# Optimization experiments

Measured on AMD Instinct MI355X. Metric: run time of the kernel, lower is better.

Reference implementation:

```python
import jax, jax.numpy as jnp
from jax import lax
import numpy as np

IMGSIZE = (360, 640)  # (H, W)
SIGMA = 71.0
LEVEL = 5
FACTOR = 2.0

_k1 = np.array([1., 4., 6., 4., 1.], dtype=np.float32) / 16.0
K5 = np.outer(_k1, _k1)  # 5x5 binomial (Gaussian) pyramid kernel


def _blur(x, scale=1.0):
    # x: (B,C,H,W); depthwise 5x5 Gaussian blur with reflect padding
    C = x.shape[1]
    xp = jnp.pad(x, ((0, 0), (0, 0), (2, 2), (2, 2)), mode='reflect')
    k = jnp.broadcast_to(jnp.asarray(K5 * scale, x.dtype), (C, 1, 5, 5))
    return lax.conv_general_dilated(xp, k, (1, 1), 'VALID',
                                    feature_group_count=C,
                                    dimension_numbers=('NCHW', 'OIHW', 'NCHW'))


def pyrdown(x):
    # OpenCV-style pyrDown: blur then drop every other row/col -> ceil(H/2), ceil(W/2)
    return _blur(x)[:, :, ::2, ::2]


def pyrup(x):
    # OpenCV-style pyrUp: zero-insertion upsample then blur with 4*kernel
    B, C, H, W = x.shape
    up = jnp.zeros((B, C, 2 * H, 2 * W), x.dtype).at[:, :, ::2, ::2].set(x)
    return _blur(up, scale=4.0)


def resize_nearest(x, h, w):
    # matches torch F.interpolate(mode='nearest'): src = floor(dst * in/out)
    H, W = x.shape[-2], x.shape[-1]
    ri = jnp.arange(h) * H // h
    ci = jnp.arange(w) * W // w
    return x[..., ri[:, None], ci[None, :]]


def _create_filter(height, width, sigma):
    s = 2.0 * sigma * sigma
    xc = int(round(width * 0.5))
    yc = int(round(height * 0.5))
    ex = jnp.arange(-xc, width - xc - 1, dtype=jnp.float32)   # (W-1,)
    ey = jnp.arange(-yc, height - yc - 1, dtype=jnp.float32)  # (H-1,)
    d = ex[:, None] ** 2 + ey[None, :] ** 2                   # (W-1, H-1)
    g = jnp.exp(-d / s)
    return (g / g.max()).T                                    # (H-1, W-1)


def _pyramid_filters():
    f = _create_filter(int(FACTOR * IMGSIZE[0]), int(FACTOR * IMGSIZE[1]), SIGMA)
    filters = [f]
    for _ in range(LEVEL):
        filters.append(pyrdown(filters[-1][None, None])[0, 0])
    return filters


def setup_inputs():
    key = jax.random.key(0)
    k1, k2 = jax.random.split(key)
    B, C = 32, 3
    H, W = IMGSIZE
    images = jax.random.normal(k1, (B, C, H, W), jnp.float32)
    u = jax.random.uniform(k2, (B, 2), jnp.float32)
    # fixations are (x, y) pixel coordinates inside the image
    fixations = u * jnp.array([W - 1.0, H - 1.0], jnp.float32)
    return {"images": images, "fixations": fixations}


def reference(images, fixations):
    filters = _pyramid_filters()
    # Laplacian pyramid construction
    pyr, cur = [], images
    up = images
    for _ in range(LEVEL):
        dn = pyrdown(cur)
        up = resize_nearest(pyrup(dn), cur.shape[2], cur.shape[3])
        pyr.append(cur - up)
        cur = dn
    fovea = up  # smallest level, upsampled back (im_smallest)
    for i in range(LEVEL - 1, -1, -1):
        f = filters[i]
        fh, fw = f.shape
        ih, iw = pyr[i].shape[2], pyr[i].shape[3]
        fix = fixations / (2.0 ** i)
        # rect = filter_size/2 - fix, truncated to int (same as torch .to(int64))
        x1 = (fw / 2.0 - fix[:, 0]).astype(jnp.int32)
        y1 = (fh / 2.0 - fix[:, 1]).astype(jnp.int32)
        # per-sample dynamic crop of size (ih, iw); crop size == target size so
        # the original's F.interpolate on the crop is the identity
        crop = jax.vmap(lambda yy, xx: lax.dynamic_slice(f, (yy, xx), (ih, iw)))(y1, x1)
        filtered = pyr[i] * crop[:, None, :, :]
        if i != LEVEL - 1:
            fovea = resize_nearest(pyrup(fovea), ih, iw)
        fovea = fovea + filtered
    return fovea
```

## Files before the change

kernel.cpp:

```cpp
#include <hip/hip_runtime.h>
#include <cstddef>


static __device__ __forceinline__ int refl(int e, int n) {
  if (e < 0) e = -e;
  if (e >= n) e = 2 * n - 2 - e;
  return e;
}

static __device__ __forceinline__ float4 loadu4(const float* p) {
  float4 v; __builtin_memcpy(&v, p, sizeof(float4)); return v;
}

static __device__ void filt_build(float* pool, float* __restrict__ fyg,
                                  float* __restrict__ fxg) {
  float* sy = pool;
  float* sx = pool + 1394;
  const int oy[5] = {0, 719, 1079, 1259, 1349};
  const int ny[5] = {719, 360, 180, 90, 45};
  const int ox[5] = {0, 1279, 1919, 2239, 2399};
  const int nx[5] = {1279, 640, 320, 160, 80};
  int tid = threadIdx.y * 64 + threadIdx.x;
  for (int i = tid; i < 719; i += 256) {
    float d = (float)(i - 360); sy[i] = expf(-d * d / 10082.0f);
  }
  for (int i = tid; i < 1279; i += 256) {
    float d = (float)(i - 640); sx[i] = expf(-d * d / 10082.0f);
  }
  __syncthreads();
  const float k0 = 0.0625f, k1 = 0.25f, k2 = 0.375f;
#pragma unroll
  for (int l = 1; l < 5; ++l) {
    const float* py = sy + oy[l - 1]; float* qy = sy + oy[l];
    int n = ny[l - 1];
    for (int i = tid; i < ny[l]; i += 256) {
      qy[i] = k0 * (py[refl(2 * i - 2, n)] + py[refl(2 * i + 2, n)]) +
              k1 * (py[refl(2 * i - 1, n)] + py[refl(2 * i + 1, n)]) +
              k2 * py[2 * i];
    }
    const float* px = sx + ox[l - 1]; float* qx = sx + ox[l];
    int m = nx[l - 1];
    for (int i = tid; i < nx[l]; i += 256) {
      qx[i] = k0 * (px[refl(2 * i - 2, m)] + px[refl(2 * i + 2, m)]) +
              k1 * (px[refl(2 * i - 1, m)] + px[refl(2 * i + 1, m)]) +
              k2 * px[2 * i];
    }
    __syncthreads();
  }
  for (int i = tid; i < 1394; i += 256) fyg[i] = sy[i];
  for (int i = tid; i < 2479; i += 256) fxg[i] = sx[i];
}

__global__ __launch_bounds__(256) void pyrdown_lds_k(
    const float* __restrict__ src, float* __restrict__ dst,
    int H, int W, int oH, int oW, int NP,
    float* __restrict__ fyo, float* __restrict__ fxo) {
  __shared__ float pool[35 * 68 * 2];
  int tx = threadIdx.x;
  int ty = threadIdx.y;
  int p  = blockIdx.z;
  if (p >= NP) {
    if (blockIdx.x == 0 && blockIdx.y == 0 && fyo) filt_build(pool, fyo, fxo);
    return;
  }
  float* te = pool;
  float* to_ = pool + 35 * 68;
  int x0 = blockIdx.x * 64;
  int Yb = blockIdx.y;
  const float* s = src + (size_t)p * H * W;
  float* d = dst + (size_t)p * oH * oW;

  int cols = min(64, oW - x0);
  int nq   = (cols + 4) >> 1;
  int gr0  = 32 * Yb - 2;
  int gc0  = 2 * x0 - 4;
  int tid  = ty * 64 + tx;

  auto loadq = [&](int r, int m) -> float4 {
    int gy = refl(gr0 + r, H);
    const float* row = s + (size_t)gy * W;
    int gc = gc0 + 4 * m;
    if (gc >= 0 && gc + 3 < W) return *(const float4*)(row + gc);
    float4 v;
    v.x = row[refl(gc, W)];
    v.y = row[refl(gc + 1, W)];
    v.z = row[refl(gc + 2, W)];
    v.w = row[refl(gc + 3, W)];
    return v;
  };
  auto putq = [&](int r, int m, float4 v) {
    *(float2*)&te[r * 68 + 2 * m]  = make_float2(v.x, v.z);
    *(float2*)&to_[r * 68 + 2 * m] = make_float2(v.y, v.w);
  };

  if (nq == 34) {
    int r0 = tid / 34,          m0 = tid - 34 * r0;
    int q1 = tid + 256;  int r1 = q1 / 34, m1 = q1 - 34 * r1;
    int q2 = tid + 512;  int r2 = q2 / 34, m2 = q2 - 34 * r2;
    int q3 = tid + 768;  int r3 = q3 / 34, m3 = q3 - 34 * r3;
    int q4 = tid + 1024; int r4 = q4 / 34, m4 = q4 - 34 * r4;
    bool g4 = (q4 < 1190);
    float4 v0 = loadq(r0, m0);
    float4 v1 = loadq(r1, m1);
    float4 v2 = loadq(r2, m2);
    float4 v3 = loadq(r3, m3);
    float4 v4;
    if (g4) v4 = loadq(r4, m4);
    putq(r0, m0, v0);
    putq(r1, m1, v1);
    putq(r2, m2, v2);
    putq(r3, m3, v3);
    if (g4) putq(r4, m4, v4);
  } else {
    float4 v[9];
#pragma unroll
    for (int i = 0; i < 9; ++i) {
      int r = ty + 4 * i;
      if (r < 35 && tx < nq) v[i] = loadq(r, tx);
    }
#pragma unroll
    for (int i = 0; i < 9; ++i) {
      int r = ty + 4 * i;
      if (r < 35 && tx < nq) putq(r, tx, v[i]);
    }
  }
  __syncthreads();

  int x = x0 + tx;
  int nPairs = (oH + 1) >> 1;
  int Yp0 = 8 * Yb + 2 * ty;
  if (x < oW && Yp0 < nPairs) {
    const float k0 = 0.0625f, k1 = 0.25f, k2 = 0.375f;
    float h[11];
    int rbase = 8 * ty;
#pragma unroll
    for (int a = 0; a < 11; ++a) {
      int r = rbase + a;
      float e0 = te[r * 68 + tx + 1], e2 = te[r * 68 + tx + 2],
            e4 = te[r * 68 + tx + 3];
      float e1 = to_[r * 68 + tx + 1], e3 = to_[r * 68 + tx + 2];
      h[a] = k0 * (e0 + e4) + k1 * (e1 + e3) + k2 * e2;
    }
    float o0 = k0 * (h[0] + h[4])  + k1 * (h[1] + h[3])  + k2 * h[2];
    float o1 = k0 * (h[2] + h[6])  + k1 * (h[3] + h[5])  + k2 * h[4];
    float o2 = k0 * (h[4] + h[8])  + k1 * (h[5] + h[7])  + k2 * h[6];
    float o3 = k0 * (h[6] + h[10]) + k1 * (h[7] + h[9])  + k2 * h[8];
    int oy0 = 2 * Yp0;
    float* drow = d + (size_t)oy0 * oW + x;
    drow[0] = o0;
    if (oy0 + 1 < oH) drow[(size_t)oW] = o1;
    if (oy0 + 2 < oH) drow[(size_t)2 * oW] = o2;
    if (oy0 + 3 < oH) drow[(size_t)3 * oW] = o3;
  }
}

static __device__ __forceinline__ float pyrdown_at(const float* c, int H, int W,
                                                   int y, int x) {
  const float k0 = 0.0625f, k1 = 0.25f, k2 = 0.375f;
  int c0 = refl(2 * x - 2, W), c1 = refl(2 * x - 1, W), c2 = 2 * x,
      c3 = refl(2 * x + 1, W), c4 = refl(2 * x + 2, W);
  float h[5];
#pragma unroll
  for (int r = 0; r < 5; ++r) {
    int gy = refl(2 * y - 2 + r, H);
    const float* row = c + gy * W;
    h[r] = k0 * (row[c0] + row[c4]) + k1 * (row[c1] + row[c3]) + k2 * row[c2];
  }
  return k0 * (h[0] + h[4]) + k1 * (h[1] + h[3]) + k2 * h[2];
}

static __device__ __forceinline__ float pyrup_at(const float* c, int Hc, int Wc,
                                                 int y, int x) {
  const float w0 = 0.125f, w1 = 0.75f;
  int yc = y >> 1, xc = x >> 1;
  if (y & 1) {
    int yb = (yc == Hc - 1) ? Hc - 1 : yc + 1;
    const float* ra = c + yc * Wc;
    const float* rb = c + yb * Wc;
    if (x & 1) {
      int xb = (xc == Wc - 1) ? Wc - 1 : xc + 1;
      return 0.25f * (ra[xc] + ra[xb] + rb[xc] + rb[xb]);
    } else {
      int xm = (xc == 0) ? 1 : xc - 1, xp = (xc == Wc - 1) ? Wc - 1 : xc + 1;
      float a = w1 * ra[xc] + w0 * (ra[xm] + ra[xp]);
      float b = w1 * rb[xc] + w0 * (rb[xm] + rb[xp]);
      return 0.5f * (a + b);
    }
  } else {
    int ym = (yc == 0) ? 1 : yc - 1, yp = (yc == Hc - 1) ? Hc - 1 : yc + 1;
    const float* rm = c + ym * Wc;
    const float* rc = c + yc * Wc;
    const float* rp = c + yp * Wc;
    if (x & 1) {
      int xb = (xc == Wc - 1) ? Wc - 1 : xc + 1;
      float a = 0.5f * (rm[xc] + rm[xb]);
      float b = 0.5f * (rc[xc] + rc[xb]);
      float e = 0.5f * (rp[xc] + rp[xb]);
      return w1 * b + w0 * (a + e);
    } else {
      int xm = (xc == 0) ? 1 : xc - 1, xp = (xc == Wc - 1) ? Wc - 1 : xc + 1;
      float a = w1 * rm[xc] + w0 * (rm[xm] + rm[xp]);
      float b = w1 * rc[xc] + w0 * (rc[xm] + rc[xp]);
      float e = w1 * rp[xc] + w0 * (rp[xm] + rp[xp]);
      return w1 * b + w0 * (a + e);
    }
  }
}

__global__ __launch_bounds__(256) void tail_k(
    const float* __restrict__ dn3, const float* __restrict__ fix,
    const float* __restrict__ fy3, const float* __restrict__ fx3,
    const float* __restrict__ fy4, const float* __restrict__ fx4,
    float* __restrict__ fv3) {
  __shared__ float c3[45 * 80];
  __shared__ float c4[23 * 40];
  __shared__ float c5[12 * 20];
  __shared__ float g4[23 * 40];
  int p = blockIdx.x;
  int tid = threadIdx.x;
  const float* src = dn3 + (size_t)p * 3600;
  for (int i = tid; i < 900; i += 256)
    ((float4*)c3)[i] = ((const float4*)src)[i];
  __syncthreads();
  for (int i = tid; i < 23 * 40; i += 256) {
    int y = i / 40, x = i - 40 * y;
    c4[i] = pyrdown_at(c3, 45, 80, y, x);
  }
  __syncthreads();
  for (int i = tid; i < 12 * 20; i += 256) {
    int y = i / 20, x = i - 20 * y;
    c5[i] = pyrdown_at(c4, 23, 40, y, x);
  }
  __syncthreads();
  int b = p / 3;
  float fxv = fix[2 * b + 0], fyv = fix[2 * b + 1];
  {
    int x1 = (int)(40.0f - fxv * 0.0625f);
    int y1 = (int)(22.5f - fyv * 0.0625f);
    for (int i = tid; i < 23 * 40; i += 256) {
      int y = i / 40, x = i - 40 * y;
      float u = pyrup_at(c5, 12, 20, y, x);
      g4[i] = u + (c4[i] - u) * (fy4[y1 + y] * fx4[x1 + x]);
    }
  }
  __syncthreads();
  {
    int x1 = (int)(80.0f - fxv * 0.125f);
    int y1 = (int)(45.0f - fyv * 0.125f);
    float* dst = fv3 + (size_t)p * 3600;
    for (int i = tid; i < 45 * 80; i += 256) {
      int y = i / 80, x = i - 80 * y;
      float uf = pyrup_at(g4, 23, 40, y, x);
      float ud = pyrup_at(c4, 23, 40, y, x);
      dst[i] = uf + (c3[i] - ud) * (fy3[y1 + y] * fx3[x1 + x]);
    }
  }
}

__global__ __launch_bounds__(256) void recon_fused_k(
    const float* __restrict__ images, const float* __restrict__ dn1,
    const float* __restrict__ dn2, const float* __restrict__ dn3,
    const float* __restrict__ fv3g, const float* __restrict__ fyg,
    const float* __restrict__ fxg, const float* __restrict__ fix,
    float* __restrict__ out) {
  __shared__ float dn1t[670], fv1t[670];
  __shared__ float dn2t[296], fv2t[296];
  __shared__ float dn3t[126], fv3t[126];
  const int bx = blockIdx.x, by = blockIdx.y, p = blockIdx.z;
  const int tid = threadIdx.x;

  const int R1r = max(8 * by - 1, 0),  R1hi = min(8 * by + 8, 179);
  const int C1r = max(64 * bx - 1, 0), C1hi = min(64 * bx + 64, 319);
  const int n1r = R1hi - R1r + 1, n1c = C1hi - C1r + 1;
  const int yc_lo = R1r >> 1, yc_hi = R1hi >> 1;
  const int xc_lo = C1r >> 1, xc_hi = C1hi >> 1;
  const int R2r = max(yc_lo - 1, 0),  R2hi = min(yc_hi + 1, 89);
  const int C2r = max(xc_lo - 1, 0),  C2hi = min(xc_hi + 1, 159);
  const int n2r = R2hi - R2r + 1, n2c = C2hi - C2r + 1;
  const int yc3_lo = R2r >> 1, yc3_hi = R2hi >> 1;
  const int xc3_lo = C2r >> 1, xc3_hi = C2hi >> 1;
  const int R3r = max(yc3_lo - 1, 0), R3hi = min(yc3_hi + 1, 44);
  const int C3r = max(xc3_lo - 1, 0), C3hi = min(xc3_hi + 1, 79);
  const int n3r = R3hi - R3r + 1, n3c = C3hi - C3r + 1;

  const float* d1p = dn1 + (size_t)p * 57600;
  const float* d2p = dn2 + (size_t)p * 14400;
  const float* d3p = dn3 + (size_t)p * 3600;
  const float* f3p = fv3g + (size_t)p * 3600;

  for (int s = tid; s < 670; s += 256) {
    int r = s / 67, c = s - 67 * r;
    if (r < n1r && c < n1c)
      dn1t[s] = d1p[(R1r + r) * 320 + (C1r + c)];
  }
  for (int s = tid; s < 296; s += 256) {
    int r = s / 37, c = s - 37 * r;
    if (r < n2r && c < n2c)
      dn2t[s] = d2p[(R2r + r) * 160 + (C2r + c)];
  }
  if (tid < 126) {
    int r = tid / 21, c = tid - 21 * r;
    if (r < n3r && c < n3c) {
      int o = (R3r + r) * 80 + (C3r + c);
      dn3t[tid] = d3p[o];
      fv3t[tid] = f3p[o];
    }
  }
  __syncthreads();

  int b = p / 3;
  float fxv = fix[2 * b + 0], fyv = fix[2 * b + 1];
  int y1_2 = (int)(90.0f - fyv * 0.25f), x1_2 = (int)(160.0f - fxv * 0.25f);
  int y1_1 = (int)(180.0f - fyv * 0.5f), x1_1 = (int)(320.0f - fxv * 0.5f);
  int y1_0 = (int)(359.5f - fyv),        x1_0 = (int)(639.5f - fxv);
  const float* fy2 = fyg + 1079; const float* fx2 = fxg + 1919;
  const float* fy1 = fyg + 719;  const float* fx1 = fxg + 1279;
  const float w0 = 0.125f, w1 = 0.75f;

  {
    int nx3 = xc3_hi - xc3_lo + 1;
    int ncell = (yc3_hi - yc3_lo + 1) * nx3;
    if (tid < ncell) {
      int cy = tid / nx3;
      int yc = yc3_lo + cy, xc = xc3_lo + (tid - cy * nx3);
      int aa0 = ((yc == 0) ? 1 : yc - 1) - R3r;
      int aa1 = yc - R3r;
      int aa2 = ((yc == 44) ? 44 : yc + 1) - R3r;
      int xm = ((xc == 0) ? 1 : xc - 1) - C3r;
      int xq = xc - C3r;
      int xp = ((xc == 79) ? 79 : xc + 1) - C3r;
      int aa[3] = {aa0, aa1, aa2};
      float heF[3], hoF[3], heD[3], hoD[3];
#pragma unroll
      for (int j = 0; j < 3; ++j) {
        const float* rf = fv3t + aa[j] * 21;
        float fm = rf[xm], fc = rf[xq], fp = rf[xp];
        heF[j] = w1 * fc + w0 * (fm + fp);
        hoF[j] = 0.5f * (fc + fp);
        const float* rd = dn3t + aa[j] * 21;
        float em = rd[xm], ec = rd[xq], ep = rd[xp];
        heD[j] = w1 * ec + w0 * (em + ep);
        hoD[j] = 0.5f * (ec + ep);
      }
      float uF[4] = {w1 * heF[1] + w0 * (heF[0] + heF[2]),
                     w1 * hoF[1] + w0 * (hoF[0] + hoF[2]),
                     0.5f * (heF[1] + heF[2]),
                     0.5f * (hoF[1] + hoF[2])};
      float uD[4] = {w1 * heD[1] + w0 * (heD[0] + heD[2]),
                     w1 * hoD[1] + w0 * (hoD[0] + hoD[2]),
                     0.5f * (heD[1] + heD[2]),
                     0.5f * (hoD[1] + hoD[2])};
      int y2 = 2 * yc, x2 = 2 * xc;
#pragma unroll
      for (int q = 0; q < 4; ++q) {
        int y = y2 + (q >> 1), x = x2 + (q & 1);
        if (y >= R2r && y <= R2hi && x >= C2r && x <= C2hi) {
          int idx = (y - R2r) * 37 + (x - C2r);
          float w = fy2[y1_2 + y] * fx2[x1_2 + x];
          fv2t[idx] = uF[q] + (dn2t[idx] - uD[q]) * w;
        }
      }
    }
  }
  __syncthreads();

  {
    int nx2 = xc_hi - xc_lo + 1;
    int ncell = (yc_hi - yc_lo + 1) * nx2;
    if (tid < ncell) {
      int cy = tid / nx2;
      int yc = yc_lo + cy, xc = xc_lo + (tid - cy * nx2);
      int aa0 = ((yc == 0) ? 1 : yc - 1) - R2r;
      int aa1 = yc - R2r;
      int aa2 = ((yc == 89) ? 89 : yc + 1) - R2r;
      int xm = ((xc == 0) ? 1 : xc - 1) - C2r;
      int xq = xc - C2r;
      int xp = ((xc == 159) ? 159 : xc + 1) - C2r;
      int aa[3] = {aa0, aa1, aa2};
      float heF[3], hoF[3], heD[3], hoD[3];
#pragma unroll
      for (int j = 0; j < 3; ++j) {
        const float* rf = fv2t + aa[j] * 37;
        float fm = rf[xm], fc = rf[xq], fp = rf[xp];
        heF[j] = w1 * fc + w0 * (fm + fp);
        hoF[j] = 0.5f * (fc + fp);
        const float* rd = dn2t + aa[j] * 37;
        float em = rd[xm], ec = rd[xq], ep = rd[xp];
        heD[j] = w1 * ec + w0 * (em + ep);
        hoD[j] = 0.5f * (ec + ep);
      }
      float uF[4] = {w1 * heF[1] + w0 * (heF[0] + heF[2]),
                     w1 * hoF[1] + w0 * (hoF[0] + hoF[2]),
                     0.5f * (heF[1] + heF[2]),
                     0.5f * (hoF[1] + hoF[2])};
      float uD[4] = {w1 * heD[1] + w0 * (heD[0] + heD[2]),
                     w1 * hoD[1] + w0 * (hoD[0] + hoD[2]),
                     0.5f * (heD[1] + heD[2]),
                     0.5f * (hoD[1] + hoD[2])};
      int y2 = 2 * yc, x2 = 2 * xc;
#pragma unroll
      for (int q = 0; q < 4; ++q) {
        int y = y2 + (q >> 1), x = x2 + (q & 1);
        if (y >= R1r && y <= R1hi && x >= C1r && x <= C1hi) {
          int idx = (y - R1r) * 67 + (x - C1r);
          float w = fy1[y1_1 + y] * fx1[x1_1 + x];
          fv1t[idx] = uF[q] + (dn1t[idx] - uD[q]) * w;
        }
      }
    }
  }
  __syncthreads();

  int trow = tid >> 5;
  int tk   = tid & 31;
  int Y = 8 * by + trow;
  if (Y >= 180) return;
  int c0 = 64 * bx + 2 * tk;
  int ry[3];
  ry[0] = ((Y == 0) ? 1 : Y - 1) - R1r;
  ry[1] = Y - R1r;
  ry[2] = ((Y == 179) ? 179 : Y + 1) - R1r;
  int cm = ((c0 == 0) ? 1 : c0 - 1) - C1r;
  int cc = c0 - C1r;
  int cp = ((c0 + 2 >= 320) ? 319 : c0 + 2) - C1r;

  float dm[3], da[3], db[3], dq[3], em[3], ea[3], eb[3], eq[3];
#pragma unroll
  for (int r = 0; r < 3; ++r) {
    const float* qd = dn1t + ry[r] * 67;
    dm[r] = qd[cm]; da[r] = qd[cc]; db[r] = qd[cc + 1]; dq[r] = qd[cp];
    const float* qe = fv1t + ry[r] * 67;
    em[r] = qe[cm]; ea[r] = qe[cc]; eb[r] = qe[cc + 1]; eq[r] = qe[cp];
  }

  float heA[3], hoA[3], heB[3], hoB[3];
#pragma unroll
  for (int r = 0; r < 3; ++r) {
    heA[r] = w1 * da[r] + w0 * (dm[r] + db[r]);
    hoA[r] = 0.5f * (da[r] + db[r]);
    heB[r] = w1 * db[r] + w0 * (da[r] + dq[r]);
    hoB[r] = 0.5f * (db[r] + dq[r]);
  }
  float u00 = w1 * heA[1] + w0 * (heA[0] + heA[2]);
  float u01 = w1 * hoA[1] + w0 * (hoA[0] + hoA[2]);
  float u02 = w1 * heB[1] + w0 * (heB[0] + heB[2]);
  float u03 = w1 * hoB[1] + w0 * (hoB[0] + hoB[2]);
  float u10 = 0.5f * (heA[1] + heA[2]);
  float u11 = 0.5f * (hoA[1] + hoA[2]);
  float u12 = 0.5f * (heB[1] + heB[2]);
  float u13 = 0.5f * (hoB[1] + hoB[2]);

  float geA[3], goA[3], geB[3], goB[3];
#pragma unroll
  for (int r = 0; r < 3; ++r) {
    geA[r] = w1 * ea[r] + w0 * (em[r] + eb[r]);
    goA[r] = 0.5f * (ea[r] + eb[r]);
    geB[r] = w1 * eb[r] + w0 * (ea[r] + eq[r]);
    goB[r] = 0.5f * (eb[r] + eq[r]);
  }
  float f00 = w1 * geA[1] + w0 * (geA[0] + geA[2]);
  float f01 = w1 * goA[1] + w0 * (goA[0] + goA[2]);
  float f02 = w1 * geB[1] + w0 * (geB[0] + geB[2]);
  float f03 = w1 * goB[1] + w0 * (goB[0] + goB[2]);
  float f10 = 0.5f * (geA[1] + geA[2]);
  float f11 = 0.5f * (goA[1] + goA[2]);
  float f12 = 0.5f * (geB[1] + geB[2]);
  float f13 = 0.5f * (goB[1] + goB[2]);

  int oy = 2 * Y, ox = 2 * c0;
  const float* crow = images + (size_t)p * 230400 + (size_t)oy * 640 + ox;
  float* orow = out + (size_t)p * 230400 + (size_t)oy * 640 + ox;
  float fyA = fyg[y1_0 + oy], fyB = fyg[y1_0 + oy + 1];
  float4 fxq = loadu4(fxg + (x1_0 + ox));

  float4 cv = *(const float4*)crow;
  float4 r0v;
  r0v.x = f00 + (cv.x - u00) * (fyA * fxq.x);
  r0v.y = f01 + (cv.y - u01) * (fyA * fxq.y);
  r0v.z = f02 + (cv.z - u02) * (fyA * fxq.z);
  r0v.w = f03 + (cv.w - u03) * (fyA * fxq.w);
  *(float4*)orow = r0v;
  float4 cv1 = *(const float4*)(crow + 640);
  float4 r1v;
  r1v.x = f10 + (cv1.x - u10) * (fyB * fxq.x);
  r1v.y = f11 + (cv1.y - u11) * (fyB * fxq.y);
  r1v.z = f12 + (cv1.z - u12) * (fyB * fxq.z);
  r1v.w = f13 + (cv1.w - u13) * (fyB * fxq.w);
  *(float4*)(orow + 640) = r1v;
}

extern "C" void kernel_launch(void* const* d_in, const int* in_sizes, int n_in,
                              void* d_out, int out_size, void* d_ws, size_t ws_size,
                              hipStream_t stream) {
  const float* images = (const float*)d_in[0];
  const float* fix    = (const float*)d_in[1];
  float* out = (float*)d_out;
  float* ws  = (float*)d_ws;

  const int P = 96;

  size_t off = 0;
  auto alloc = [&](size_t n) { float* p = ws + off; off += (n + 3) & ~(size_t)3; return p; };
  float* fyg = alloc(1394);
  float* fxg = alloc(2479);
  float* dn1 = alloc((size_t)P * 180 * 320);
  float* dn2 = alloc((size_t)P * 90 * 160);
  float* dn3 = alloc((size_t)P * 45 * 80);
  float* fv3 = alloc((size_t)P * 45 * 80);
  if (ws_size < off * sizeof(float)) return;

  dim3 blk(64, 4, 1);
  auto pgrd = [](int oW, int oH, int p) {
    int nPairs = (oH + 1) / 2;
    return dim3((unsigned)((oW + 63) / 64), (unsigned)((nPairs + 7) / 8), (unsigned)p);
  };

  pyrdown_lds_k<<<pgrd(320, 180, P + 1), blk, 0, stream>>>(
      images, dn1, 360, 640, 180, 320, P, fyg, fxg);
  pyrdown_lds_k<<<pgrd(160, 90, P), blk, 0, stream>>>(
      dn1, dn2, 180, 320, 90, 160, P, nullptr, nullptr);
  pyrdown_lds_k<<<pgrd(80, 45, P), blk, 0, stream>>>(
      dn2, dn3, 90, 160, 45, 80, P, nullptr, nullptr);

  tail_k<<<dim3(P), dim3(256), 0, stream>>>(
      dn3, fix, fyg + 1259, fxg + 2239, fyg + 1349, fxg + 2399, fv3);

  recon_fused_k<<<dim3(5, 23, P), dim3(256), 0, stream>>>(
      images, dn1, dn2, dn3, fv3, fyg, fxg, fix, out);
}
```

Baseline: 231.7 us.

## Fuse third pyrdown into tail kernel and enlarge recon tiles to 32 rows

The third pyramid-down level is now computed inside tail_k from dn2 staged in LDS, which removes one kernel launch and a global round trip. Each recon_fused_k block now covers 32 level-1 rows instead of 8, so halo overlap is smaller and there are fewer blocks. Each thread walks 4 rows with a sliding three-row register window, and global loads are batched into registers before the LDS writes. In exchange, tail_k uses about 74KB of LDS with only 96 blocks, which serialises work on few CUs, and recon has far fewer blocks.

```diff
diff --git a/kernel.cpp b/kernel.cpp
--- a/kernel.cpp
+++ b/kernel.cpp
@@ -208,19 +208,28 @@
 }
 
 __global__ __launch_bounds__(256) void tail_k(
-    const float* __restrict__ dn3, const float* __restrict__ fix,
+    const float* __restrict__ dn2g, const float* __restrict__ fix,
     const float* __restrict__ fy3, const float* __restrict__ fx3,
     const float* __restrict__ fy4, const float* __restrict__ fx4,
-    float* __restrict__ fv3) {
+    float* __restrict__ dn3g, float* __restrict__ fv3) {
+  __shared__ float s2[90 * 160];
   __shared__ float c3[45 * 80];
   __shared__ float c4[23 * 40];
   __shared__ float c5[12 * 20];
   __shared__ float g4[23 * 40];
   int p = blockIdx.x;
   int tid = threadIdx.x;
-  const float* src = dn3 + (size_t)p * 3600;
-  for (int i = tid; i < 900; i += 256)
-    ((float4*)c3)[i] = ((const float4*)src)[i];
+  const float* src = dn2g + (size_t)p * 14400;
+  for (int i = tid; i < 3600; i += 256)
+    ((float4*)s2)[i] = ((const float4*)src)[i];
+  __syncthreads();
+  float* d3 = dn3g + (size_t)p * 3600;
+  for (int i = tid; i < 3600; i += 256) {
+    int y = i / 80, x = i - 80 * y;
+    float v = pyrdown_at(s2, 90, 160, y, x);
+    c3[i] = v;
+    d3[i] = v;
+  }
   __syncthreads();
   for (int i = tid; i < 23 * 40; i += 256) {
     int y = i / 40, x = i - 40 * y;
@@ -263,14 +272,14 @@
     const float* __restrict__ fv3g, const float* __restrict__ fyg,
     const float* __restrict__ fxg, const float* __restrict__ fix,
     float* __restrict__ out) {
-  __shared__ float dn1t[670], fv1t[670];
-  __shared__ float dn2t[296], fv2t[296];
-  __shared__ float dn3t[126], fv3t[126];
+  __shared__ float dn1t[2278], fv1t[2278];
+  __shared__ float dn2t[740],  fv2t[740];
+  __shared__ float dn3t[252],  fv3t[252];
   const int bx = blockIdx.x, by = blockIdx.y, p = blockIdx.z;
   const int tid = threadIdx.x;
 
-  const int R1r = max(8 * by - 1, 0),  R1hi = min(8 * by + 8, 179);
-  const int C1r = max(64 * bx - 1, 0), C1hi = min(64 * bx + 64, 319);
+  const int R1r = max(32 * by - 1, 0),  R1hi = min(32 * by + 32, 179);
+  const int C1r = max(64 * bx - 1, 0),  C1hi = min(64 * bx + 64, 319);
   const int n1r = R1hi - R1r + 1, n1c = C1hi - C1r + 1;
   const int yc_lo = R1r >> 1, yc_hi = R1hi >> 1;
   const int xc_lo = C1r >> 1, xc_hi = C1hi >> 1;
@@ -288,23 +297,45 @@
   const float* d3p = dn3 + (size_t)p * 3600;
   const float* f3p = fv3g + (size_t)p * 3600;
 
-  for (int s = tid; s < 670; s += 256) {
-    int r = s / 67, c = s - 67 * r;
-    if (r < n1r && c < n1c)
-      dn1t[s] = d1p[(R1r + r) * 320 + (C1r + c)];
-  }
-  for (int s = tid; s < 296; s += 256) {
-    int r = s / 37, c = s - 37 * r;
-    if (r < n2r && c < n2c)
-      dn2t[s] = d2p[(R2r + r) * 160 + (C2r + c)];
-  }
-  if (tid < 126) {
-    int r = tid / 21, c = tid - 21 * r;
-    if (r < n3r && c < n3c) {
-      int o = (R3r + r) * 80 + (C3r + c);
-      dn3t[tid] = d3p[o];
-      fv3t[tid] = f3p[o];
-    }
+  {
+    float v1[9];
+#pragma unroll
+    for (int it = 0; it < 9; ++it) {
+      int s = tid + 256 * it;
+      if (s < 2278) {
+        int r = s / 67, c = s - 67 * r;
+        if (r < n1r && c < n1c) v1[it] = d1p[(R1r + r) * 320 + (C1r + c)];
+      }
+    }
+    float v2[3];
+#pragma unroll
+    for (int it = 0; it < 3; ++it) {
+      int s = tid + 256 * it;
+      if (s < 740) {
+        int r = s / 37, c = s - 37 * r;
+        if (r < n2r && c < n2c) v2[it] = d2p[(R2r + r) * 160 + (C2r + c)];
+      }
+    }
+    float v3a = 0.f, v3b = 0.f;
+    if (tid < 252) {
+      int r = tid / 21, c = tid - 21 * r;
+      if (r < n3r && c < n3c) {
+        int o = (R3r + r) * 80 + (C3r + c);
+        v3a = d3p[o];
+        v3b = f3p[o];
+      }
+    }
+#pragma unroll
+    for (int it = 0; it < 9; ++it) {
+      int s = tid + 256 * it;
+      if (s < 2278) dn1t[s] = v1[it];
+    }
+#pragma unroll
+    for (int it = 0; it < 3; ++it) {
+      int s = tid + 256 * it;
+      if (s < 740) dn2t[s] = v2[it];
+    }
+    if (tid < 252) { dn3t[tid] = v3a; fv3t[tid] = v3b; }
   }
   __syncthreads();
 
@@ -318,18 +349,18 @@
   const float w0 = 0.125f, w1 = 0.75f;
 
   {
-    int nx3 = xc3_hi - xc3_lo + 1;
-    int ncell = (yc3_hi - yc3_lo + 1) * nx3;
+    int nxa = xc3_hi - xc3_lo + 1;
+    int ncell = (yc3_hi - yc3_lo + 1) * nxa;
     if (tid < ncell) {
-      int cy = tid / nx3;
-      int yc = yc3_lo + cy, xc = xc3_lo + (tid - cy * nx3);
-      int aa0 = ((yc == 0) ? 1 : yc - 1) - R3r;
-      int aa1 = yc - R3r;
-      int aa2 = ((yc == 44) ? 44 : yc + 1) - R3r;
+      int cy = tid / nxa;
+      int yc = yc3_lo + cy, xc = xc3_lo + (tid - cy * nxa);
+      int a0 = ((yc == 0) ? 1 : yc - 1) - R3r;
+      int a1 = yc - R3r;
+      int a2 = ((yc == 44) ? 44 : yc + 1) - R3r;
       int xm = ((xc == 0) ? 1 : xc - 1) - C3r;
       int xq = xc - C3r;
       int xp = ((xc == 79) ? 79 : xc + 1) - C3r;
-      int aa[3] = {aa0, aa1, aa2};
+      int aa[3] = {a0, a1, a2};
       float heF[3], hoF[3], heD[3], hoD[3];
 #pragma unroll
       for (int j = 0; j < 3; ++j) {
@@ -365,18 +396,18 @@
   __syncthreads();
 
   {
-    int nx2 = xc_hi - xc_lo + 1;
-    int ncell = (yc_hi - yc_lo + 1) * nx2;
-    if (tid < ncell) {
-      int cy = tid / nx2;
-      int yc = yc_lo + cy, xc = xc_lo + (tid - cy * nx2);
-      int aa0 = ((yc == 0) ? 1 : yc - 1) - R2r;
-      int aa1 = yc - R2r;
-      int aa2 = ((yc == 89) ? 89 : yc + 1) - R2r;
+    int nxb = xc_hi - xc_lo + 1;
+    int ncell = (yc_hi - yc_lo + 1) * nxb;
+    for (int s = tid; s < ncell; s += 256) {
+      int cy = s / nxb;
+      int yc = yc_lo + cy, xc = xc_lo + (s - cy * nxb);
+      int a0 = ((yc == 0) ? 1 : yc - 1) - R2r;
+      int a1 = yc - R2r;
+      int a2 = ((yc == 89) ? 89 : yc + 1) - R2r;
       int xm = ((xc == 0) ? 1 : xc - 1) - C2r;
       int xq = xc - C2r;
       int xp = ((xc == 159) ? 159 : xc + 1) - C2r;
-      int aa[3] = {aa0, aa1, aa2};
+      int aa[3] = {a0, a1, a2};
       float heF[3], hoF[3], heD[3], hoD[3];
 #pragma unroll
       for (int j = 0; j < 3; ++j) {
@@ -411,82 +442,80 @@
   }
   __syncthreads();
 
-  int trow = tid >> 5;
-  int tk   = tid & 31;
-  int Y = 8 * by + trow;
-  if (Y >= 180) return;
+  int tg = tid >> 5;
+  int tk = tid & 31;
+  int Y0 = 32 * by + 4 * tg;
+  if (Y0 > 179) return;
   int c0 = 64 * bx + 2 * tk;
-  int ry[3];
-  ry[0] = ((Y == 0) ? 1 : Y - 1) - R1r;
-  ry[1] = Y - R1r;
-  ry[2] = ((Y == 179) ? 179 : Y + 1) - R1r;
   int cm = ((c0 == 0) ? 1 : c0 - 1) - C1r;
   int cc = c0 - C1r;
   int cp = ((c0 + 2 >= 320) ? 319 : c0 + 2) - C1r;
 
-  float dm[3], da[3], db[3], dq[3], em[3], ea[3], eb[3], eq[3];
-#pragma unroll
-  for (int r = 0; r < 3; ++r) {
-    const float* qd = dn1t + ry[r] * 67;
-    dm[r] = qd[cm]; da[r] = qd[cc]; db[r] = qd[cc + 1]; dq[r] = qd[cp];
-    const float* qe = fv1t + ry[r] * 67;
-    em[r] = qe[cm]; ea[r] = qe[cc]; eb[r] = qe[cc + 1]; eq[r] = qe[cp];
-  }
-
-  float heA[3], hoA[3], heB[3], hoB[3];
-#pragma unroll
-  for (int r = 0; r < 3; ++r) {
-    heA[r] = w1 * da[r] + w0 * (dm[r] + db[r]);
-    hoA[r] = 0.5f * (da[r] + db[r]);
-    heB[r] = w1 * db[r] + w0 * (da[r] + dq[r]);
-    hoB[r] = 0.5f * (db[r] + dq[r]);
-  }
-  float u00 = w1 * heA[1] + w0 * (heA[0] + heA[2]);
-  float u01 = w1 * hoA[1] + w0 * (hoA[0] + hoA[2]);
-  float u02 = w1 * heB[1] + w0 * (heB[0] + heB[2]);
-  float u03 = w1 * hoB[1] + w0 * (hoB[0] + hoB[2]);
-  float u10 = 0.5f * (heA[1] + heA[2]);
-  float u11 = 0.5f * (hoA[1] + hoA[2]);
-  float u12 = 0.5f * (heB[1] + heB[2]);
-  float u13 = 0.5f * (hoB[1] + hoB[2]);
-
-  float geA[3], goA[3], geB[3], goB[3];
-#pragma unroll
-  for (int r = 0; r < 3; ++r) {
-    geA[r] = w1 * ea[r] + w0 * (em[r] + eb[r]);
-    goA[r] = 0.5f * (ea[r] + eb[r]);
-    geB[r] = w1 * eb[r] + w0 * (ea[r] + eq[r]);
-    goB[r] = 0.5f * (eb[r] + eq[r]);
-  }
-  float f00 = w1 * geA[1] + w0 * (geA[0] + geA[2]);
-  float f01 = w1 * goA[1] + w0 * (goA[0] + goA[2]);
-  float f02 = w1 * geB[1] + w0 * (geB[0] + geB[2]);
-  float f03 = w1 * goB[1] + w0 * (goB[0] + goB[2]);
-  float f10 = 0.5f * (geA[1] + geA[2]);
-  float f11 = 0.5f * (goA[1] + goA[2]);
-  float f12 = 0.5f * (geB[1] + geB[2]);
-  float f13 = 0.5f * (goB[1] + goB[2]);
-
-  int oy = 2 * Y, ox = 2 * c0;
-  const float* crow = images + (size_t)p * 230400 + (size_t)oy * 640 + ox;
-  float* orow = out + (size_t)p * 230400 + (size_t)oy * 640 + ox;
-  float fyA = fyg[y1_0 + oy], fyB = fyg[y1_0 + oy + 1];
+  struct Hrow { float dAe, dAo, dBe, dBo, fAe, fAo, fBe, fBo; };
+  auto loadrow = [&](int j) -> Hrow {
+    int rr = Y0 - 1 + j;
+    rr = (rr < 0) ? 1 : (rr > 179 ? 179 : rr);
+    const float* qd = dn1t + (rr - R1r) * 67;
+    const float* qe = fv1t + (rr - R1r) * 67;
+    float d0 = qd[cm], d1 = qd[cc], d2 = qd[cc + 1], d3v = qd[cp];
+    float e0 = qe[cm], e1 = qe[cc], e2 = qe[cc + 1], e3v = qe[cp];
+    Hrow h;
+    h.dAe = w1 * d1 + w0 * (d0 + d2);  h.dAo = 0.5f * (d1 + d2);
+    h.dBe = w1 * d2 + w0 * (d1 + d3v); h.dBo = 0.5f * (d2 + d3v);
+    h.fAe = w1 * e1 + w0 * (e0 + e2);  h.fAo = 0.5f * (e1 + e2);
+    h.fBe = w1 * e2 + w0 * (e1 + e3v); h.fBo = 0.5f * (e2 + e3v);
+    return h;
+  };
+
+  Hrow hp = loadrow(0), hc = loadrow(1), hn = loadrow(2);
+  int ox = 2 * c0;
+  const float* ibase = images + (size_t)p * 230400 + ox;
+  float* obase = out + (size_t)p * 230400 + ox;
   float4 fxq = loadu4(fxg + (x1_0 + ox));
 
-  float4 cv = *(const float4*)crow;
-  float4 r0v;
-  r0v.x = f00 + (cv.x - u00) * (fyA * fxq.x);
-  r0v.y = f01 + (cv.y - u01) * (fyA * fxq.y);
-  r0v.z = f02 + (cv.z - u02) * (fyA * fxq.z);
-  r0v.w = f03 + (cv.w - u03) * (fyA * fxq.w);
-  *(float4*)orow = r0v;
-  float4 cv1 = *(const float4*)(crow + 640);
-  float4 r1v;
-  r1v.x = f10 + (cv1.x - u10) * (fyB * fxq.x);
-  r1v.y = f11 + (cv1.y - u11) * (fyB * fxq.y);
-  r1v.z = f12 + (cv1.z - u12) * (fyB * fxq.z);
-  r1v.w = f13 + (cv1.w - u13) * (fyB * fxq.w);
-  *(float4*)(orow + 640) = r1v;
+#pragma unroll
+  for (int i = 0; i < 4; ++i) {
+    int Y = Y0 + i;
+    if (Y <= 179) {
+      float u00 = w1 * hc.dAe + w0 * (hp.dAe + hn.dAe);
+      float u01 = w1 * hc.dAo + w0 * (hp.dAo + hn.dAo);
+      float u02 = w1 * hc.dBe + w0 * (hp.dBe + hn.dBe);
+      float u03 = w1 * hc.dBo + w0 * (hp.dBo + hn.dBo);
+      float u10 = 0.5f * (hc.dAe + hn.dAe);
+      float u11 = 0.5f * (hc.dAo + hn.dAo);
+      float u12 = 0.5f * (hc.dBe + hn.dBe);
+      float u13 = 0.5f * (hc.dBo + hn.dBo);
+      float f00 = w1 * hc.fAe + w0 * (hp.fAe + hn.fAe);
+      float f01 = w1 * hc.fAo + w0 * (hp.fAo + hn.fAo);
+      float f02 = w1 * hc.fBe + w0 * (hp.fBe + hn.fBe);
+      float f03 = w1 * hc.fBo + w0 * (hp.fBo + hn.fBo);
+      float f10 = 0.5f * (hc.fAe + hn.fAe);
+      float f11 = 0.5f * (hc.fAo + hn.fAo);
+      float f12 = 0.5f * (hc.fBe + hn.fBe);
+      float f13 = 0.5f * (hc.fBo + hn.fBo);
+
+      int oy = 2 * Y;
+      const float* crow = ibase + (size_t)oy * 640;
+      float* orow = obase + (size_t)oy * 640;
+      float fyA = fyg[y1_0 + oy], fyB = fyg[y1_0 + oy + 1];
+
+      float4 cv = *(const float4*)crow;
+      float4 r0v;
+      r0v.x = f00 + (cv.x - u00) * (fyA * fxq.x);
+      r0v.y = f01 + (cv.y - u01) * (fyA * fxq.y);
+      r0v.z = f02 + (cv.z - u02) * (fyA * fxq.z);
+      r0v.w = f03 + (cv.w - u03) * (fyA * fxq.w);
+      *(float4*)orow = r0v;
+      float4 cv1 = *(const float4*)(crow + 640);
+      float4 r1v;
+      r1v.x = f10 + (cv1.x - u10) * (fyB * fxq.x);
+      r1v.y = f11 + (cv1.y - u11) * (fyB * fxq.y);
+      r1v.z = f12 + (cv1.z - u12) * (fyB * fxq.z);
+      r1v.w = f13 + (cv1.w - u13) * (fyB * fxq.w);
+      *(float4*)(orow + 640) = r1v;
+    }
+    if (i < 3) { hp = hc; hc = hn; hn = loadrow(i + 3); }
+  }
 }
 
 extern "C" void kernel_launch(void* const* d_in, const int* in_sizes, int n_in,
@@ -519,12 +548,10 @@
       images, dn1, 360, 640, 180, 320, P, fyg, fxg);
   pyrdown_lds_k<<<pgrd(160, 90, P), blk, 0, stream>>>(
       dn1, dn2, 180, 320, 90, 160, P, nullptr, nullptr);
-  pyrdown_lds_k<<<pgrd(80, 45, P), blk, 0, stream>>>(
-      dn2, dn3, 90, 160, 45, 80, P, nullptr, nullptr);
 
   tail_k<<<dim3(P), dim3(256), 0, stream>>>(
-      dn3, fix, fyg + 1259, fxg + 2239, fyg + 1349, fxg + 2399, fv3);
-
-  recon_fused_k<<<dim3(5, 23, P), dim3(256), 0, stream>>>(
+      dn2, fix, fyg + 1259, fxg + 2239, fyg + 1349, fxg + 2399, dn3, fv3);
+
+  recon_fused_k<<<dim3(5, 6, P), dim3(256), 0, stream>>>(
       images, dn1, dn2, dn3, fv3, fyg, fxg, fix, out);
 }
```

Result: faster. 223.1 us (-3.7%).
